# Performance work log

Hardware: AMD Instinct MI355X
Metric: run time of the kernel (lower is better)

The kernel has to match this reference:

```python
import jax, jax.numpy as jnp
import numpy as np

INPUT_DIM = 64

def setup_inputs() -> dict:
    key = jax.random.key(0)
    k1, k2, k3 = jax.random.split(key, 3)
    B, Lq, Lk, D = 4, 4096, 4096, INPUT_DIM
    return {
        "query": jax.random.normal(k1, (B, Lq, D), dtype=jnp.float32),
        "keys": jax.random.normal(k2, (B, Lk, D), dtype=jnp.float32),
        "values": jax.random.normal(k3, (B, Lk, D), dtype=jnp.float32),
    }

def reference(query, keys, values):
    scale = 1.0 / jnp.sqrt(jnp.asarray(INPUT_DIM, dtype=jnp.float32))
    # scores: [B, Lq, Lk]
    scores = jnp.einsum("bqd,bkd->bqk", query, keys) * scale
    attn = jax.nn.softmax(scores, axis=-1)
    # output: [B, Lq, D]
    return jnp.einsum("bqk,bkd->bqd", attn, values)
```

## Files before the change

kernel.cpp:

```cpp
#include <hip/hip_runtime.h>
#include <hip/hip_bf16.h>

typedef __bf16 bf16x8 __attribute__((ext_vector_type(8)));
typedef float  f32x4  __attribute__((ext_vector_type(4)));

#define LQ 4096
#define LKK 4096
#define DH 64
#define KBLK 64
#define QBLK 64
#define NIT (LKK / KBLK)
#define NB 4
#define GR_TILE 512
#define ARR_ELEMS ((size_t)NB * NIT * GR_TILE * 8)
#define KV_BYTES (4 * ARR_ELEMS * sizeof(__bf16))
#define PO_BYTES ((size_t)512 * 4096 * sizeof(float))
#define PML_BYTES ((size_t)512 * 128 * sizeof(float))
#define WS_SPLIT (KV_BYTES + PO_BYTES + PML_BYTES)
#define WS_SINGLE KV_BYTES

union BFU { unsigned short u; __bf16 b; };
__device__ __forceinline__ __bf16 u2bf(unsigned short v) { BFU x; x.u = v; return x.b; }
__device__ __forceinline__ unsigned short bf2u(__bf16 b) { BFU x; x.b = b; return x.u; }

typedef const __attribute__((address_space(1))) void* gas1_t;
typedef __attribute__((address_space(3))) void* las3_t;
__device__ __forceinline__ void gload_lds16(const void* g, void* l) {
    __builtin_amdgcn_global_load_lds((gas1_t)g, (las3_t)l, 16, 0, 0);
}


__global__ __launch_bounds__(256)
void prepack(const float* __restrict__ Kg, const float* __restrict__ Vg,
             __bf16* __restrict__ ws)
{
    __bf16* KHI = ws;
    __bf16* KLO = ws + ARR_ELEMS;
    __bf16* VHI = ws + 2 * ARR_ELEMS;
    __bf16* VLO = ws + 3 * ARR_ELEMS;

    const int gid = blockIdx.x * 256 + threadIdx.x;
    const int isV = gid >> 17;
    const int t   = gid & 131071;
    const int b   = t >> 15;
    const int rem = t & 32767;
    const int kt  = rem >> 9;
    const int G   = rem & 511;
    const int blk = G >> 7;
    const int c   = (G >> 6) & 1;
    const int gg  = (G >> 4) & 3;
    const int ll  = G & 15;

    const size_t dst = ((size_t)(b * NIT + kt) * GR_TILE + G) * 8;
    float x[8];
    if (!isV) {
        const float* src = Kg + ((size_t)b * LKK + kt * KBLK + 16 * blk + ll) * DH + 32 * c + 8 * gg;
        float4 a0 = *(const float4*)src;
        float4 a1 = *(const float4*)(src + 4);
        x[0]=a0.x; x[1]=a0.y; x[2]=a0.z; x[3]=a0.w;
        x[4]=a1.x; x[5]=a1.y; x[6]=a1.z; x[7]=a1.w;
        bf16x8 h, l;
#pragma unroll
        for (int j = 0; j < 8; ++j) {
            __bf16 hh = (__bf16)x[j];
            h[j] = hh; l[j] = (__bf16)(x[j] - (float)hh);
        }
        *(bf16x8*)&KHI[dst] = h;  *(bf16x8*)&KLO[dst] = l;
    } else {
        const float* src = Vg + ((size_t)b * LKK + kt * KBLK + 32 * c + 8 * gg) * DH + 16 * blk + ll;
#pragma unroll
        for (int j = 0; j < 8; ++j) x[j] = src[(size_t)j * DH];
        bf16x8 h, l;
#pragma unroll
        for (int j = 0; j < 8; ++j) {
            __bf16 hh = (__bf16)x[j];
            h[j] = hh; l[j] = (__bf16)(x[j] - (float)hh);
        }
        *(bf16x8*)&VHI[dst] = h;  *(bf16x8*)&VLO[dst] = l;
    }
}

__global__ __launch_bounds__(256, 2)
void attn_split(const float* __restrict__ Qg, const __bf16* __restrict__ ws,
                float* __restrict__ PO, float* __restrict__ PML)
{
    const int bid = blockIdx.x;
    const int h   = bid & 1;
    const int bz  = (bid >> 1) & 3;
    const int qt  = bid >> 3;
    const int pb  = h * 256 + bz * 64 + qt;
    const int tid  = threadIdx.x;
    const int w    = tid >> 6;
    const int lane = tid & 63;
    const int g    = lane >> 4;
    const int l15  = lane & 15;
    const int q0   = qt * QBLK + w * 16;

    __shared__ __align__(16) __bf16 TILES[2][4][GR_TILE * 8];
    __shared__ __align__(16) unsigned int PSM[4][16 * 64];

    const __bf16* wsA[4] = { ws, ws + ARR_ELEMS, ws + 2 * ARR_ELEMS, ws + 3 * ARR_ELEMS };
    const size_t bqoff = (size_t)bz * LQ * DH;

    bf16x8 qhi[2], qlo[2];
#pragma unroll
    for (int c = 0; c < 2; ++c) {
        const float* src = Qg + bqoff + (size_t)(q0 + l15) * DH + 32 * c + 8 * g;
#pragma unroll
        for (int j = 0; j < 8; ++j) {
            float x = src[j] * 0.125f;
            __bf16 hh = (__bf16)x;
            qhi[c][j] = hh;
            qlo[c][j] = (__bf16)(x - (float)hh);
        }
    }

    auto STAGE = [&](int buf, int kt) {
        const size_t toff = (size_t)(bz * NIT + kt) * GR_TILE * 8;
#pragma unroll
        for (int a = 0; a < 4; ++a) {
            const __bf16* src = wsA[a] + toff + (size_t)(w * 128 + lane) * 8;
            __bf16* dst = &TILES[buf][a][w * 128 * 8];
            gload_lds16(src, dst);
            gload_lds16(src + 64 * 8, dst + 64 * 8);
        }
    };

    f32x4 oacc[4] = {};
    float m_run[4], l_run[4];
#pragma unroll
    for (int r = 0; r < 4; ++r) { m_run[r] = -1e30f; l_run[r] = 0.f; }

    const int kt0 = h * (NIT / 2);
    STAGE(0, kt0);
    __syncthreads();

    int cur = 0;
    for (int it = 0; it < NIT / 2; ++it) {
        if (it + 1 < NIT / 2) STAGE(cur ^ 1, kt0 + it + 1);

        const __bf16* KHI_l = TILES[cur][0];
        const __bf16* KLO_l = TILES[cur][1];
        const __bf16* VHI_l = TILES[cur][2];
        const __bf16* VLO_l = TILES[cur][3];

        f32x4 s[4] = {};
        __builtin_amdgcn_s_setprio(1);
#pragma unroll
        for (int kb = 0; kb < 4; ++kb) {
#pragma unroll
            for (int c = 0; c < 2; ++c) {
                bf16x8 kh = *(const bf16x8*)&KHI_l[((kb * 2 + c) * 64 + lane) * 8];
                bf16x8 kl = *(const bf16x8*)&KLO_l[((kb * 2 + c) * 64 + lane) * 8];
                s[kb] = __builtin_amdgcn_mfma_f32_16x16x32_bf16(qhi[c], kh, s[kb], 0, 0, 0);
                s[kb] = __builtin_amdgcn_mfma_f32_16x16x32_bf16(qlo[c], kh, s[kb], 0, 0, 0);
                s[kb] = __builtin_amdgcn_mfma_f32_16x16x32_bf16(qhi[c], kl, s[kb], 0, 0, 0);
            }
        }
        __builtin_amdgcn_s_setprio(0);

        float tmax[4];
#pragma unroll
        for (int r = 0; r < 4; ++r)
            tmax[r] = fmaxf(fmaxf(s[0][r], s[1][r]), fmaxf(s[2][r], s[3][r]));
#pragma unroll
        for (int off = 1; off < 16; off <<= 1)
#pragma unroll
            for (int r = 0; r < 4; ++r)
                tmax[r] = fmaxf(tmax[r], __shfl_xor(tmax[r], off, 64));

        float alpha[4], psum[4];
#pragma unroll
        for (int r = 0; r < 4; ++r) {
            float mnew = fmaxf(m_run[r], tmax[r]);
            alpha[r] = __expf(m_run[r] - mnew);
            m_run[r] = mnew;
            psum[r] = 0.f;
        }
#pragma unroll
        for (int kb = 0; kb < 4; ++kb)
#pragma unroll
            for (int r = 0; r < 4; ++r) {
                float p = __expf(s[kb][r] - m_run[r]);
                s[kb][r] = p;
                psum[r] += p;
            }
#pragma unroll
        for (int off = 1; off < 16; off <<= 1)
#pragma unroll
            for (int r = 0; r < 4; ++r)
                psum[r] += __shfl_xor(psum[r], off, 64);
#pragma unroll
        for (int r = 0; r < 4; ++r) {
            l_run[r] = l_run[r] * alpha[r] + psum[r];
#pragma unroll
            for (int db = 0; db < 4; ++db) oacc[db][r] *= alpha[r];
        }

#pragma unroll
        for (int kb = 0; kb < 4; ++kb)
#pragma unroll
            for (int r = 0; r < 4; ++r) {
                float p = s[kb][r];
                __bf16 hh = (__bf16)p;
                __bf16 ll2 = (__bf16)(p - (float)hh);
                const int row = 4 * g + r;
                const int idx = row * 64 + (((4 * kb + (l15 >> 2) + row) & 15) << 2) + (l15 & 3);
                PSM[w][idx] = (unsigned int)bf2u(hh) | ((unsigned int)bf2u(ll2) << 16);
            }

#pragma unroll
        for (int c = 0; c < 2; ++c) {
            const unsigned int* prow = &PSM[w][l15 * 64];
            const int qg = 2 * g + 8 * c;
            uint4 ulo = *(const uint4*)&prow[((qg + l15) & 15) << 2];
            uint4 uhi = *(const uint4*)&prow[((qg + 1 + l15) & 15) << 2];
            unsigned int uu[8] = { ulo.x, ulo.y, ulo.z, ulo.w, uhi.x, uhi.y, uhi.z, uhi.w };
            bf16x8 ph, pl;
#pragma unroll
            for (int j = 0; j < 8; ++j) {
                ph[j] = u2bf((unsigned short)(uu[j] & 0xffffu));
                pl[j] = u2bf((unsigned short)(uu[j] >> 16));
            }
            __builtin_amdgcn_s_setprio(1);
#pragma unroll
            for (int db = 0; db < 4; ++db) {
                bf16x8 vh = *(const bf16x8*)&VHI_l[((db * 2 + c) * 64 + lane) * 8];
                bf16x8 vl = *(const bf16x8*)&VLO_l[((db * 2 + c) * 64 + lane) * 8];
                oacc[db] = __builtin_amdgcn_mfma_f32_16x16x32_bf16(ph, vh, oacc[db], 0, 0, 0);
                oacc[db] = __builtin_amdgcn_mfma_f32_16x16x32_bf16(ph, vl, oacc[db], 0, 0, 0);
                oacc[db] = __builtin_amdgcn_mfma_f32_16x16x32_bf16(pl, vh, oacc[db], 0, 0, 0);
            }
            __builtin_amdgcn_s_setprio(0);
        }

        __syncthreads();
        cur ^= 1;
    }

    float* po = PO + (size_t)pb * (QBLK * DH);
    const int rbase = w * 16;
#pragma unroll
    for (int r = 0; r < 4; ++r)
#pragma unroll
        for (int db = 0; db < 4; ++db)
            po[(rbase + 4 * g + r) * DH + 16 * db + l15] = oacc[db][r];
    if (l15 == 0) {
#pragma unroll
        for (int r = 0; r < 4; ++r) {
            PML[pb * 128 + rbase + 4 * g + r]      = m_run[r];
            PML[pb * 128 + 64 + rbase + 4 * g + r] = l_run[r];
        }
    }
}

__global__ __launch_bounds__(256)
void combine(const float* __restrict__ PO, const float* __restrict__ PML,
             float* __restrict__ Og)
{
    const int t  = blockIdx.x * 256 + threadIdx.x;
    const int d   = t & 63;
    const int row = (t >> 6) & 4095;
    const int bz  = t >> 18;
    const int qt  = row >> 6, ri = row & 63;
    const int pb0 = bz * 64 + qt;
    const int pb1 = 256 + pb0;
    float m0 = PML[pb0 * 128 + ri], l0 = PML[pb0 * 128 + 64 + ri];
    float m1 = PML[pb1 * 128 + ri], l1 = PML[pb1 * 128 + 64 + ri];
    float M  = fmaxf(m0, m1);
    float a0 = __expf(m0 - M), a1 = __expf(m1 - M);
    float o0 = PO[(size_t)pb0 * 4096 + ri * 64 + d];
    float o1 = PO[(size_t)pb1 * 4096 + ri * 64 + d];
    Og[t] = (a0 * o0 + a1 * o1) / (a0 * l0 + a1 * l1);
}

__global__ __launch_bounds__(256, 1)
void attn_fwd_pre(const float* __restrict__ Qg, const __bf16* __restrict__ ws,
                  float* __restrict__ Og)
{
    const int bid = blockIdx.x;
    const int bz  = (bid >> 1) & 3;
    const int qt  = ((bid & 1) << 5) | (bid >> 3);
    const int tid  = threadIdx.x;
    const int w    = tid >> 6;
    const int lane = tid & 63;
    const int g    = lane >> 4;
    const int l15  = lane & 15;
    const int q0   = qt * QBLK + w * 16;

    __shared__ __align__(16) __bf16 TILES[2][4][GR_TILE * 8];
    __shared__ __align__(16) unsigned int PSM[4][16 * 64];

    const __bf16* wsA[4] = { ws, ws + ARR_ELEMS, ws + 2 * ARR_ELEMS, ws + 3 * ARR_ELEMS };
    const size_t bqoff = (size_t)bz * LQ * DH;

    bf16x8 qhi[2], qlo[2];
#pragma unroll
    for (int c = 0; c < 2; ++c) {
        const float* src = Qg + bqoff + (size_t)(q0 + l15) * DH + 32 * c + 8 * g;
#pragma unroll
        for (int j = 0; j < 8; ++j) {
            float x = src[j] * 0.125f;
            __bf16 hh = (__bf16)x;
            qhi[c][j] = hh;
            qlo[c][j] = (__bf16)(x - (float)hh);
        }
    }

    auto STAGE = [&](int buf, int kt) {
        const size_t toff = (size_t)(bz * NIT + kt) * GR_TILE * 8;
#pragma unroll
        for (int a = 0; a < 4; ++a) {
            const __bf16* src = wsA[a] + toff + (size_t)(w * 128 + lane) * 8;
            __bf16* dst = &TILES[buf][a][w * 128 * 8];
            gload_lds16(src, dst);
            gload_lds16(src + 64 * 8, dst + 64 * 8);
        }
    };

    f32x4 oacc[4] = {};
    float m_run[4], l_run[4];
#pragma unroll
    for (int r = 0; r < 4; ++r) { m_run[r] = -1e30f; l_run[r] = 0.f; }

    STAGE(0, 0);
    __syncthreads();

    int cur = 0;
    for (int kt = 0; kt < NIT; ++kt) {
        if (kt + 1 < NIT) STAGE(cur ^ 1, kt + 1);

        const __bf16* KHI_l = TILES[cur][0];
        const __bf16* KLO_l = TILES[cur][1];
        const __bf16* VHI_l = TILES[cur][2];
        const __bf16* VLO_l = TILES[cur][3];

        f32x4 s[4] = {};
        __builtin_amdgcn_s_setprio(1);
#pragma unroll
        for (int kb = 0; kb < 4; ++kb) {
#pragma unroll
            for (int c = 0; c < 2; ++c) {
                bf16x8 kh = *(const bf16x8*)&KHI_l[((kb * 2 + c) * 64 + lane) * 8];
                bf16x8 kl = *(const bf16x8*)&KLO_l[((kb * 2 + c) * 64 + lane) * 8];
                s[kb] = __builtin_amdgcn_mfma_f32_16x16x32_bf16(qhi[c], kh, s[kb], 0, 0, 0);
                s[kb] = __builtin_amdgcn_mfma_f32_16x16x32_bf16(qlo[c], kh, s[kb], 0, 0, 0);
                s[kb] = __builtin_amdgcn_mfma_f32_16x16x32_bf16(qhi[c], kl, s[kb], 0, 0, 0);
            }
        }
        __builtin_amdgcn_s_setprio(0);

        float tmax[4];
#pragma unroll
        for (int r = 0; r < 4; ++r)
            tmax[r] = fmaxf(fmaxf(s[0][r], s[1][r]), fmaxf(s[2][r], s[3][r]));
#pragma unroll
        for (int off = 1; off < 16; off <<= 1)
#pragma unroll
            for (int r = 0; r < 4; ++r)
                tmax[r] = fmaxf(tmax[r], __shfl_xor(tmax[r], off, 64));

        float alpha[4], psum[4];
#pragma unroll
        for (int r = 0; r < 4; ++r) {
            float mnew = fmaxf(m_run[r], tmax[r]);
            alpha[r] = __expf(m_run[r] - mnew);
            m_run[r] = mnew;
            psum[r] = 0.f;
        }
#pragma unroll
        for (int kb = 0; kb < 4; ++kb)
#pragma unroll
            for (int r = 0; r < 4; ++r) {
                float p = __expf(s[kb][r] - m_run[r]);
                s[kb][r] = p;
                psum[r] += p;
            }
#pragma unroll
        for (int off = 1; off < 16; off <<= 1)
#pragma unroll
            for (int r = 0; r < 4; ++r)
                psum[r] += __shfl_xor(psum[r], off, 64);
#pragma unroll
        for (int r = 0; r < 4; ++r) {
            l_run[r] = l_run[r] * alpha[r] + psum[r];
#pragma unroll
            for (int db = 0; db < 4; ++db) oacc[db][r] *= alpha[r];
        }

#pragma unroll
        for (int kb = 0; kb < 4; ++kb)
#pragma unroll
            for (int r = 0; r < 4; ++r) {
                float p = s[kb][r];
                __bf16 hh = (__bf16)p;
                __bf16 ll2 = (__bf16)(p - (float)hh);
                const int row = 4 * g + r;
                const int idx = row * 64 + (((4 * kb + (l15 >> 2) + row) & 15) << 2) + (l15 & 3);
                PSM[w][idx] = (unsigned int)bf2u(hh) | ((unsigned int)bf2u(ll2) << 16);
            }

#pragma unroll
        for (int c = 0; c < 2; ++c) {
            const unsigned int* prow = &PSM[w][l15 * 64];
            const int qg = 2 * g + 8 * c;
            uint4 ulo = *(const uint4*)&prow[((qg + l15) & 15) << 2];
            uint4 uhi = *(const uint4*)&prow[((qg + 1 + l15) & 15) << 2];
            unsigned int uu[8] = { ulo.x, ulo.y, ulo.z, ulo.w, uhi.x, uhi.y, uhi.z, uhi.w };
            bf16x8 ph, pl;
#pragma unroll
            for (int j = 0; j < 8; ++j) {
                ph[j] = u2bf((unsigned short)(uu[j] & 0xffffu));
                pl[j] = u2bf((unsigned short)(uu[j] >> 16));
            }
            __builtin_amdgcn_s_setprio(1);
#pragma unroll
            for (int db = 0; db < 4; ++db) {
                bf16x8 vh = *(const bf16x8*)&VHI_l[((db * 2 + c) * 64 + lane) * 8];
                bf16x8 vl = *(const bf16x8*)&VLO_l[((db * 2 + c) * 64 + lane) * 8];
                oacc[db] = __builtin_amdgcn_mfma_f32_16x16x32_bf16(ph, vh, oacc[db], 0, 0, 0);
                oacc[db] = __builtin_amdgcn_mfma_f32_16x16x32_bf16(ph, vl, oacc[db], 0, 0, 0);
                oacc[db] = __builtin_amdgcn_mfma_f32_16x16x32_bf16(pl, vh, oacc[db], 0, 0, 0);
            }
            __builtin_amdgcn_s_setprio(0);
        }

        __syncthreads();
        cur ^= 1;
    }

#pragma unroll
    for (int r = 0; r < 4; ++r) {
        float inv = 1.0f / l_run[r];
#pragma unroll
        for (int db = 0; db < 4; ++db)
            Og[bqoff + (size_t)(q0 + 4 * g + r) * DH + 16 * db + l15] = oacc[db][r] * inv;
    }
}

extern "C" void kernel_launch(void* const* d_in, const int* in_sizes, int n_in,
                              void* d_out, int out_size, void* d_ws, size_t ws_size,
                              hipStream_t stream) {
    (void)in_sizes; (void)n_in; (void)out_size;
    const float* Q = (const float*)d_in[0];
    const float* K = (const float*)d_in[1];
    const float* V = (const float*)d_in[2];
    float* O = (float*)d_out;

    if (ws_size >= WS_SPLIT) {
        __bf16* ws = (__bf16*)d_ws;
        float* PO  = (float*)((char*)d_ws + KV_BYTES);
        float* PML = (float*)((char*)d_ws + KV_BYTES + PO_BYTES);
        prepack<<<dim3(1024), dim3(256), 0, stream>>>(K, V, ws);
        attn_split<<<dim3(512), dim3(256), 0, stream>>>(Q, ws, PO, PML);
        combine<<<dim3(4096), dim3(256), 0, stream>>>(PO, PML, O);
    } else if (ws_size >= WS_SINGLE) {
        __bf16* ws = (__bf16*)d_ws;
        prepack<<<dim3(1024), dim3(256), 0, stream>>>(K, V, ws);
        attn_fwd_pre<<<dim3(256), dim3(256), 0, stream>>>(Q, ws, O);
    }
}
```

Baseline: 157.5 us.

## Transpose MFMA operands in split kernel, add lazy rescale and packed bf16 conversion

In the split-K attention kernel, the MFMA operands are swapped so each lane holds one query row's scores in its accumulator. The row max and sum reductions therefore need only two cross-lane shuffles, and the softmax state becomes one scalar per lane. It adds a deferred rescale that skips the alpha multiply while the new tile max stays within 8 of the running max. It also uses v_cvt_pk_bf16_f32 for the hi/lo split, stores P with an XOR-swizzled layout that reads back as contiguous bf16x8, and writes the partial output with vectorised stores. Separately, the s_setprio hints are removed from the single-pass kernel, which may change scheduling; the deferred rescale relies on exp values staying bounded by e^8.

```diff
diff --git a/kernel.cpp b/kernel.cpp
--- a/kernel.cpp
+++ b/kernel.cpp
@@ -27,6 +27,12 @@
 typedef __attribute__((address_space(3))) void* las3_t;
 __device__ __forceinline__ void gload_lds16(const void* g, void* l) {
     __builtin_amdgcn_global_load_lds((gas1_t)g, (las3_t)l, 16, 0, 0);
+}
+
+__device__ __forceinline__ unsigned cvt_pk_bf16(float a, float b) {
+    unsigned r;
+    asm volatile("v_cvt_pk_bf16_f32 %0, %1, %2" : "=v"(r) : "v"(a), "v"(b));
+    return r;
 }
 
 
@@ -127,15 +133,16 @@
     };
 
     f32x4 oacc[4] = {};
-    float m_run[4], l_run[4];
-#pragma unroll
-    for (int r = 0; r < 4; ++r) { m_run[r] = -1e30f; l_run[r] = 0.f; }
+    float m_run = -1e30f, l_run = 0.f;
 
     const int kt0 = h * (NIT / 2);
     STAGE(0, kt0);
     __syncthreads();
 
     int cur = 0;
+    const int sw = (l15 & 7) << 2;
+    const int prow = l15 * 64;
+
     for (int it = 0; it < NIT / 2; ++it) {
         if (it + 1 < NIT / 2) STAGE(cur ^ 1, kt0 + it + 1);
 
@@ -152,84 +159,80 @@
             for (int c = 0; c < 2; ++c) {
                 bf16x8 kh = *(const bf16x8*)&KHI_l[((kb * 2 + c) * 64 + lane) * 8];
                 bf16x8 kl = *(const bf16x8*)&KLO_l[((kb * 2 + c) * 64 + lane) * 8];
-                s[kb] = __builtin_amdgcn_mfma_f32_16x16x32_bf16(qhi[c], kh, s[kb], 0, 0, 0);
-                s[kb] = __builtin_amdgcn_mfma_f32_16x16x32_bf16(qlo[c], kh, s[kb], 0, 0, 0);
-                s[kb] = __builtin_amdgcn_mfma_f32_16x16x32_bf16(qhi[c], kl, s[kb], 0, 0, 0);
+                s[kb] = __builtin_amdgcn_mfma_f32_16x16x32_bf16(kh, qhi[c], s[kb], 0, 0, 0);
+                s[kb] = __builtin_amdgcn_mfma_f32_16x16x32_bf16(kh, qlo[c], s[kb], 0, 0, 0);
+                s[kb] = __builtin_amdgcn_mfma_f32_16x16x32_bf16(kl, qhi[c], s[kb], 0, 0, 0);
             }
         }
         __builtin_amdgcn_s_setprio(0);
 
-        float tmax[4];
-#pragma unroll
-        for (int r = 0; r < 4; ++r)
-            tmax[r] = fmaxf(fmaxf(s[0][r], s[1][r]), fmaxf(s[2][r], s[3][r]));
-#pragma unroll
-        for (int off = 1; off < 16; off <<= 1)
+        float tmax = -1e30f;
+#pragma unroll
+        for (int kb = 0; kb < 4; ++kb)
 #pragma unroll
             for (int r = 0; r < 4; ++r)
-                tmax[r] = fmaxf(tmax[r], __shfl_xor(tmax[r], off, 64));
-
-        float alpha[4], psum[4];
-#pragma unroll
-        for (int r = 0; r < 4; ++r) {
-            float mnew = fmaxf(m_run[r], tmax[r]);
-            alpha[r] = __expf(m_run[r] - mnew);
-            m_run[r] = mnew;
-            psum[r] = 0.f;
-        }
+                tmax = fmaxf(tmax, s[kb][r]);
+        tmax = fmaxf(tmax, __shfl_xor(tmax, 16, 64));
+        tmax = fmaxf(tmax, __shfl_xor(tmax, 32, 64));
+
+        const bool defer = __all(tmax <= m_run + 8.f);
+        float alpha = 1.f;
+        if (!defer) {
+            float mnew = fmaxf(m_run, tmax);
+            alpha = __expf(m_run - mnew);
+            m_run = mnew;
+        }
+
+        float psum = 0.f;
 #pragma unroll
         for (int kb = 0; kb < 4; ++kb)
 #pragma unroll
             for (int r = 0; r < 4; ++r) {
-                float p = __expf(s[kb][r] - m_run[r]);
+                float p = __expf(s[kb][r] - m_run);
                 s[kb][r] = p;
-                psum[r] += p;
-            }
-#pragma unroll
-        for (int off = 1; off < 16; off <<= 1)
-#pragma unroll
-            for (int r = 0; r < 4; ++r)
-                psum[r] += __shfl_xor(psum[r], off, 64);
-#pragma unroll
-        for (int r = 0; r < 4; ++r) {
-            l_run[r] = l_run[r] * alpha[r] + psum[r];
-#pragma unroll
-            for (int db = 0; db < 4; ++db) oacc[db][r] *= alpha[r];
-        }
-
-#pragma unroll
-        for (int kb = 0; kb < 4; ++kb)
-#pragma unroll
-            for (int r = 0; r < 4; ++r) {
-                float p = s[kb][r];
-                __bf16 hh = (__bf16)p;
-                __bf16 ll2 = (__bf16)(p - (float)hh);
-                const int row = 4 * g + r;
-                const int idx = row * 64 + (((4 * kb + (l15 >> 2) + row) & 15) << 2) + (l15 & 3);
-                PSM[w][idx] = (unsigned int)bf2u(hh) | ((unsigned int)bf2u(ll2) << 16);
-            }
+                psum += p;
+            }
+        psum += __shfl_xor(psum, 16, 64);
+        psum += __shfl_xor(psum, 32, 64);
+
+        if (!defer) {
+            l_run = l_run * alpha + psum;
+#pragma unroll
+            for (int db = 0; db < 4; ++db) oacc[db] *= alpha;
+        } else {
+            l_run += psum;
+        }
+
+#pragma unroll
+        for (int kb = 0; kb < 4; ++kb) {
+            unsigned h0 = cvt_pk_bf16(s[kb][0], s[kb][1]);
+            unsigned h1 = cvt_pk_bf16(s[kb][2], s[kb][3]);
+            float l0 = s[kb][0] - __uint_as_float(h0 << 16);
+            float l1 = s[kb][1] - __uint_as_float(h0 & 0xffff0000u);
+            float l2 = s[kb][2] - __uint_as_float(h1 << 16);
+            float l3 = s[kb][3] - __uint_as_float(h1 & 0xffff0000u);
+            unsigned lo0 = cvt_pk_bf16(l0, l1);
+            unsigned lo1 = cvt_pk_bf16(l2, l3);
+            const int wb = 8 * kb + 2 * g;
+            PSM[w][prow + ((wb)     ^ sw)]      = h0;
+            PSM[w][prow + ((wb + 1) ^ sw)]      = h1;
+            PSM[w][prow + 32 + ((wb)     ^ sw)] = lo0;
+            PSM[w][prow + 32 + ((wb + 1) ^ sw)] = lo1;
+        }
 
 #pragma unroll
         for (int c = 0; c < 2; ++c) {
-            const unsigned int* prow = &PSM[w][l15 * 64];
-            const int qg = 2 * g + 8 * c;
-            uint4 ulo = *(const uint4*)&prow[((qg + l15) & 15) << 2];
-            uint4 uhi = *(const uint4*)&prow[((qg + 1 + l15) & 15) << 2];
-            unsigned int uu[8] = { ulo.x, ulo.y, ulo.z, ulo.w, uhi.x, uhi.y, uhi.z, uhi.w };
-            bf16x8 ph, pl;
-#pragma unroll
-            for (int j = 0; j < 8; ++j) {
-                ph[j] = u2bf((unsigned short)(uu[j] & 0xffffu));
-                pl[j] = u2bf((unsigned short)(uu[j] >> 16));
-            }
+            const int qb = prow + (((4 * c + g) ^ (l15 & 7)) << 2);
+            bf16x8 ph = *(const bf16x8*)&PSM[w][qb];
+            bf16x8 pl = *(const bf16x8*)&PSM[w][qb + 32];
             __builtin_amdgcn_s_setprio(1);
 #pragma unroll
             for (int db = 0; db < 4; ++db) {
                 bf16x8 vh = *(const bf16x8*)&VHI_l[((db * 2 + c) * 64 + lane) * 8];
                 bf16x8 vl = *(const bf16x8*)&VLO_l[((db * 2 + c) * 64 + lane) * 8];
-                oacc[db] = __builtin_amdgcn_mfma_f32_16x16x32_bf16(ph, vh, oacc[db], 0, 0, 0);
-                oacc[db] = __builtin_amdgcn_mfma_f32_16x16x32_bf16(ph, vl, oacc[db], 0, 0, 0);
-                oacc[db] = __builtin_amdgcn_mfma_f32_16x16x32_bf16(pl, vh, oacc[db], 0, 0, 0);
+                oacc[db] = __builtin_amdgcn_mfma_f32_16x16x32_bf16(vh, ph, oacc[db], 0, 0, 0);
+                oacc[db] = __builtin_amdgcn_mfma_f32_16x16x32_bf16(vl, ph, oacc[db], 0, 0, 0);
+                oacc[db] = __builtin_amdgcn_mfma_f32_16x16x32_bf16(vh, pl, oacc[db], 0, 0, 0);
             }
             __builtin_amdgcn_s_setprio(0);
         }
@@ -238,19 +241,13 @@
         cur ^= 1;
     }
 
-    float* po = PO + (size_t)pb * (QBLK * DH);
-    const int rbase = w * 16;
-#pragma unroll
-    for (int r = 0; r < 4; ++r)
-#pragma unroll
-        for (int db = 0; db < 4; ++db)
-            po[(rbase + 4 * g + r) * DH + 16 * db + l15] = oacc[db][r];
-    if (l15 == 0) {
-#pragma unroll
-        for (int r = 0; r < 4; ++r) {
-            PML[pb * 128 + rbase + 4 * g + r]      = m_run[r];
-            PML[pb * 128 + 64 + rbase + 4 * g + r] = l_run[r];
-        }
+    float* po = PO + (size_t)pb * (QBLK * DH) + (size_t)(w * 16 + l15) * DH;
+#pragma unroll
+    for (int db = 0; db < 4; ++db)
+        *(f32x4*)&po[16 * db + 4 * g] = oacc[db];
+    if (g == 0) {
+        PML[pb * 128 + w * 16 + l15]      = m_run;
+        PML[pb * 128 + 64 + w * 16 + l15] = l_run;
     }
 }
 
@@ -336,7 +333,6 @@
         const __bf16* VLO_l = TILES[cur][3];
 
         f32x4 s[4] = {};
-        __builtin_amdgcn_s_setprio(1);
 #pragma unroll
         for (int kb = 0; kb < 4; ++kb) {
 #pragma unroll
@@ -348,7 +344,6 @@
                 s[kb] = __builtin_amdgcn_mfma_f32_16x16x32_bf16(qhi[c], kl, s[kb], 0, 0, 0);
             }
         }
-        __builtin_amdgcn_s_setprio(0);
 
         float tmax[4];
 #pragma unroll
@@ -402,10 +397,10 @@
 
 #pragma unroll
         for (int c = 0; c < 2; ++c) {
-            const unsigned int* prow = &PSM[w][l15 * 64];
+            const unsigned int* prow2 = &PSM[w][l15 * 64];
             const int qg = 2 * g + 8 * c;
-            uint4 ulo = *(const uint4*)&prow[((qg + l15) & 15) << 2];
-            uint4 uhi = *(const uint4*)&prow[((qg + 1 + l15) & 15) << 2];
+            uint4 ulo = *(const uint4*)&prow2[((qg + l15) & 15) << 2];
+            uint4 uhi = *(const uint4*)&prow2[((qg + 1 + l15) & 15) << 2];
             unsigned int uu[8] = { ulo.x, ulo.y, ulo.z, ulo.w, uhi.x, uhi.y, uhi.z, uhi.w };
             bf16x8 ph, pl;
 #pragma unroll
@@ -413,7 +408,6 @@
                 ph[j] = u2bf((unsigned short)(uu[j] & 0xffffu));
                 pl[j] = u2bf((unsigned short)(uu[j] >> 16));
             }
-            __builtin_amdgcn_s_setprio(1);
 #pragma unroll
             for (int db = 0; db < 4; ++db) {
                 bf16x8 vh = *(const bf16x8*)&VHI_l[((db * 2 + c) * 64 + lane) * 8];
@@ -422,7 +416,6 @@
                 oacc[db] = __builtin_amdgcn_mfma_f32_16x16x32_bf16(ph, vl, oacc[db], 0, 0, 0);
                 oacc[db] = __builtin_amdgcn_mfma_f32_16x16x32_bf16(pl, vh, oacc[db], 0, 0, 0);
             }
-            __builtin_amdgcn_s_setprio(0);
         }
 
         __syncthreads();
```

Result: faster. 132.7 us (-15.7%).
